# Kernel tuning notes

Hardware: AMD Instinct MI355X
Metric: run time of the kernel (lower is better)

Reference implementation:

```python
import jax, jax.numpy as jnp
import numpy as np

N = 1_000_000
FEAT_DIM = 256
N_CLASS = 345
N_DOMAIN = 6
BETA = 0.5
EPS = 1e-5


def setup_inputs() -> dict:
    key = jax.random.key(0)
    k1, k2, k3, k4 = jax.random.split(key, 4)
    feats = jax.random.normal(k1, (N, FEAT_DIM), dtype=jnp.float32)
    mean = jax.random.normal(k2, (N_DOMAIN, N_CLASS, FEAT_DIM), dtype=jnp.float32)
    amount = jnp.zeros((N_DOMAIN, N_CLASS), dtype=jnp.float32)
    labels = jax.random.randint(k3, (N,), 0, N_CLASS, dtype=jnp.int64 if jax.config.jax_enable_x64 else jnp.int32)
    domains = jax.random.randint(k4, (N,), 0, N_DOMAIN, dtype=jnp.int64 if jax.config.jax_enable_x64 else jnp.int32)
    return {"feats": feats, "mean": mean, "amount": amount,
            "labels": labels, "domains": domains}


def reference(feats, mean, amount, labels, domains):
    # Segmented per-(domain, class) mean of feats. Equivalent to the original
    # onehot broadcast-multiply + sum, but without the O(N*C*F) intermediate.
    seg = domains * N_CLASS + labels  # [N]
    sums = jax.ops.segment_sum(feats, seg, num_segments=N_DOMAIN * N_CLASS)
    sums = sums.reshape(N_DOMAIN, N_CLASS, FEAT_DIM)
    counts = jax.ops.segment_sum(jnp.ones((feats.shape[0],), dtype=feats.dtype), seg,
                                 num_segments=N_DOMAIN * N_CLASS)
    counts = counts.reshape(N_DOMAIN, N_CLASS)

    tmp_mean = sums / (counts[..., None] + EPS)  # [D, C, F]
    # Mask of (domain, class) cells actually observed (tmp_mean row nonzero)
    tmp_mask = (jnp.sum(tmp_mean, axis=-1) != 0).astype(feats.dtype)[..., None]  # [D, C, 1]

    new_mean = mean * (1.0 - tmp_mask) + (mean * BETA + tmp_mean * (1.0 - BETA)) * tmp_mask
    new_amount = jnp.where(counts > 0, jnp.ones_like(amount), amount)
    return new_mean, new_amount
```

## Files before the change

### kernel.cpp

```cpp
#include <hip/hip_runtime.h>
#include <stddef.h>

constexpr int FEAT = 256;
constexpr int F4   = FEAT / 4;
constexpr int NCLS = 345;
constexpr int NDOM = 6;
constexpr int NSEG = NCLS * NDOM;
constexpr int SB   = 256;
constexpr int NTAIL = 22;
constexpr int NFULL = NSEG - NTAIL;
constexpr float BETA = 0.5f;
constexpr float EPS  = 1e-5f;

typedef float f32x4 __attribute__((ext_vector_type(4)));

__global__ void __launch_bounds__(256)
k_hist(const int* __restrict__ labels, const int* __restrict__ domains,
       int n, int chunk, int* __restrict__ W) {
    __shared__ int h[NSEG];
    for (int i = threadIdx.x; i < NSEG; i += blockDim.x) h[i] = 0;
    __syncthreads();
    const int b  = blockIdx.x;
    const int lo = b * chunk;
    const int hi = min(n, lo + chunk);
    for (int i = lo + threadIdx.x; i < hi; i += blockDim.x) {
        int s = domains[i] * NCLS + labels[i];
        atomicAdd(&h[s], 1);
    }
    __syncthreads();
    int* Wb = W + (size_t)b * NSEG;
    for (int i = threadIdx.x; i < NSEG; i += blockDim.x) Wb[i] = h[i];
}

__global__ void __launch_bounds__(256)
k_bases_tot(const int* __restrict__ W, int* __restrict__ Bmat,
            int* __restrict__ totals) {
    const int s = blockIdx.x;
    const int t = threadIdx.x;
    __shared__ int sc[SB];
    int w = W[(size_t)t * NSEG + s];
    sc[t] = w;
    __syncthreads();
    for (int off = 1; off < SB; off <<= 1) {
        int v = (t >= off) ? sc[t - off] : 0;
        __syncthreads();
        sc[t] += v;
        __syncthreads();
    }
    Bmat[(size_t)t * NSEG + s] = sc[t] - w;
    if (t == SB - 1) totals[s] = sc[t];
}

__global__ void k_scan(const int* __restrict__ totals, int* __restrict__ offsets) {
    constexpr int T  = 256;
    constexpr int CH = (NSEG + T - 1) / T;
    __shared__ int csum[T];
    int t = threadIdx.x;
    int base = t * CH;
    int sum = 0;
    for (int j = 0; j < CH; ++j) {
        int idx = base + j;
        if (idx < NSEG) sum += totals[idx];
    }
    csum[t] = sum;
    __syncthreads();
    for (int off = 1; off < T; off <<= 1) {
        int v = (t >= off) ? csum[t - off] : 0;
        __syncthreads();
        csum[t] += v;
        __syncthreads();
    }
    int run = csum[t] - sum;
    for (int j = 0; j < CH; ++j) {
        int idx = base + j;
        if (idx < NSEG) {
            offsets[idx] = run;
            run += totals[idx];
        }
    }
}

__global__ void __launch_bounds__(256)
k_scatter(const int* __restrict__ labels, const int* __restrict__ domains,
          int n, int chunk, const int* __restrict__ Bmat,
          const int* __restrict__ offsets, int* __restrict__ sorted) {
    __shared__ int cur[NSEG];
    const int b = blockIdx.x;
    const int* Bb = Bmat + (size_t)b * NSEG;
    for (int i = threadIdx.x; i < NSEG; i += blockDim.x) cur[i] = Bb[i] + offsets[i];
    __syncthreads();
    const int lo = b * chunk;
    const int hi = min(n, lo + chunk);
    for (int i = lo + threadIdx.x; i < hi; i += blockDim.x) {
        int s = domains[i] * NCLS + labels[i];
        int pos = atomicAdd(&cur[s], 1);
        sorted[pos] = i;
    }
}

__global__ void __launch_bounds__(256)
k_reduce_mixed(const float* __restrict__ feats, const float* __restrict__ mean,
               const float* __restrict__ amount, const int* __restrict__ sorted,
               const int* __restrict__ totals, const int* __restrict__ offsets,
               float* __restrict__ partial, float* __restrict__ out) {
    const int b = blockIdx.x;
    int seg, lo, hi, pslot = 0;
    if (b < NFULL) {
        seg = b;
        lo = 0;
        hi = totals[seg];
    } else {
        const int j  = b - NFULL;
        seg = NFULL + (j >> 2);
        const int q  = j & 3;
        const int cnt = totals[seg];
        const int cq  = (cnt + 3) >> 2;
        lo = min(cnt, q * cq);
        hi = min(cnt, lo + cq);
        pslot = j;
    }
    const int qn   = hi - lo;
    const int base = offsets[seg] + lo;
    const int lane = threadIdx.x & 63;
    const int rp   = threadIdx.x >> 6;

    f32x4 acc = (f32x4)0.0f;
    int r = rp;
    for (; r + 28 < qn; r += 32) {
        int i0 = sorted[base + r];
        int i1 = sorted[base + r + 4];
        int i2 = sorted[base + r + 8];
        int i3 = sorted[base + r + 12];
        int i4 = sorted[base + r + 16];
        int i5 = sorted[base + r + 20];
        int i6 = sorted[base + r + 24];
        int i7 = sorted[base + r + 28];
        f32x4 v0 = reinterpret_cast<const f32x4*>(feats + (size_t)i0 * FEAT)[lane];
        f32x4 v1 = reinterpret_cast<const f32x4*>(feats + (size_t)i1 * FEAT)[lane];
        f32x4 v2 = reinterpret_cast<const f32x4*>(feats + (size_t)i2 * FEAT)[lane];
        f32x4 v3 = reinterpret_cast<const f32x4*>(feats + (size_t)i3 * FEAT)[lane];
        f32x4 v4 = reinterpret_cast<const f32x4*>(feats + (size_t)i4 * FEAT)[lane];
        f32x4 v5 = reinterpret_cast<const f32x4*>(feats + (size_t)i5 * FEAT)[lane];
        f32x4 v6 = reinterpret_cast<const f32x4*>(feats + (size_t)i6 * FEAT)[lane];
        f32x4 v7 = reinterpret_cast<const f32x4*>(feats + (size_t)i7 * FEAT)[lane];
        acc += (v0 + v1) + (v2 + v3) + ((v4 + v5) + (v6 + v7));
    }
    for (; r < qn; r += 4) {
        int i0 = sorted[base + r];
        acc += reinterpret_cast<const f32x4*>(feats + (size_t)i0 * FEAT)[lane];
    }

    __shared__ f32x4 sh[4][F4];
    sh[rp][lane] = acc;
    __syncthreads();
    if (rp == 0) {
        f32x4 s = acc + sh[1][lane] + sh[2][lane] + sh[3][lane];
        if (b < NFULL) {
            const int cnt = hi;
            float inv = 1.0f / ((float)cnt + EPS);
            f32x4 tm = s * inv;
            float lsum = tm.x + tm.y + tm.z + tm.w;
            for (int off = 1; off < 64; off <<= 1) lsum += __shfl_xor(lsum, off, 64);
            bool msk = (lsum != 0.0f);
            f32x4 m4 = reinterpret_cast<const f32x4*>(mean)[(size_t)seg * F4 + lane];
            f32x4 o = msk ? (m4 * BETA + tm * (1.0f - BETA)) : m4;
            reinterpret_cast<f32x4*>(out)[(size_t)seg * F4 + lane] = o;
            if (lane == 0) {
                out[(size_t)NSEG * FEAT + seg] = (cnt > 0) ? 1.0f : amount[seg];
            }
        } else {
            reinterpret_cast<f32x4*>(partial)[(size_t)pslot * F4 + lane] = s;
        }
    }
}

__global__ void k_final_tail(const float* __restrict__ partial, const float* __restrict__ mean,
                             const float* __restrict__ amount, const int* __restrict__ totals,
                             float* __restrict__ out) {
    const int ts   = blockIdx.x;
    const int seg  = NFULL + ts;
    const int lane = threadIdx.x;
    const int cnt  = totals[seg];
    const f32x4* P = reinterpret_cast<const f32x4*>(partial);
    f32x4 s = P[(size_t)(4 * ts + 0) * F4 + lane]
            + P[(size_t)(4 * ts + 1) * F4 + lane]
            + P[(size_t)(4 * ts + 2) * F4 + lane]
            + P[(size_t)(4 * ts + 3) * F4 + lane];
    float inv = 1.0f / ((float)cnt + EPS);
    f32x4 tm = s * inv;

    float lsum = tm.x + tm.y + tm.z + tm.w;
    for (int off = 1; off < 64; off <<= 1) lsum += __shfl_xor(lsum, off, 64);
    bool msk = (lsum != 0.0f);

    f32x4 m4 = reinterpret_cast<const f32x4*>(mean)[(size_t)seg * F4 + lane];
    f32x4 o = msk ? (m4 * BETA + tm * (1.0f - BETA)) : m4;
    reinterpret_cast<f32x4*>(out)[(size_t)seg * F4 + lane] = o;
    if (lane == 0) {
        out[(size_t)NSEG * FEAT + seg] = (cnt > 0) ? 1.0f : amount[seg];
    }
}

__global__ void k_fb_zero(float* __restrict__ out, int total) {
    int stride = gridDim.x * blockDim.x;
    for (int i = blockIdx.x * blockDim.x + threadIdx.x; i < total; i += stride) out[i] = 0.f;
}

__global__ void k_fb_acc(const float* __restrict__ feats, const int* __restrict__ labels,
                         const int* __restrict__ domains, int n, float* __restrict__ out) {
    int lane   = threadIdx.x & 63;
    int gwave  = (blockIdx.x * blockDim.x + threadIdx.x) >> 6;
    int nwaves = (gridDim.x * blockDim.x) >> 6;
    for (int i = gwave; i < n; i += nwaves) {
        int seg = domains[i] * NCLS + labels[i];
        const float4 v = reinterpret_cast<const float4*>(feats + (size_t)i * FEAT)[lane];
        float* dst = out + (size_t)seg * FEAT + lane * 4;
        atomicAdd(dst + 0, v.x);
        atomicAdd(dst + 1, v.y);
        atomicAdd(dst + 2, v.z);
        atomicAdd(dst + 3, v.w);
        if (lane == 0) atomicAdd(out + (size_t)NSEG * FEAT + seg, 1.0f);
    }
}

__global__ void k_fb_epi(const float* __restrict__ mean, const float* __restrict__ amount,
                         float* __restrict__ out) {
    int seg  = blockIdx.x;
    int lane = threadIdx.x;
    float cntf = out[(size_t)NSEG * FEAT + seg];
    float4 s = reinterpret_cast<float4*>(out)[(size_t)seg * F4 + lane];
    float inv = 1.0f / (cntf + EPS);
    float4 tm = make_float4(s.x * inv, s.y * inv, s.z * inv, s.w * inv);
    float lsum = tm.x + tm.y + tm.z + tm.w;
    for (int off = 1; off < 64; off <<= 1) lsum += __shfl_xor(lsum, off, 64);
    bool msk = (lsum != 0.0f);
    float4 m4 = reinterpret_cast<const float4*>(mean)[(size_t)seg * F4 + lane];
    float4 o;
    if (msk) {
        o.x = m4.x * BETA + tm.x * (1.f - BETA);
        o.y = m4.y * BETA + tm.y * (1.f - BETA);
        o.z = m4.z * BETA + tm.z * (1.f - BETA);
        o.w = m4.w * BETA + tm.w * (1.f - BETA);
    } else {
        o = m4;
    }
    reinterpret_cast<float4*>(out)[(size_t)seg * F4 + lane] = o;
    if (lane == 0) {
        out[(size_t)NSEG * FEAT + seg] = (cntf > 0.5f) ? 1.0f : amount[seg];
    }
}

extern "C" void kernel_launch(void* const* d_in, const int* in_sizes, int n_in,
                              void* d_out, int out_size, void* d_ws, size_t ws_size,
                              hipStream_t stream) {
    const float* feats   = (const float*)d_in[0];
    const float* mean    = (const float*)d_in[1];
    const float* amount  = (const float*)d_in[2];
    const int*   labels  = (const int*)d_in[3];
    const int*   domains = (const int*)d_in[4];
    float* out = (float*)d_out;
    const int n = in_sizes[3];
    const int chunk = (n + SB - 1) / SB;

    size_t need = ((size_t)n + (size_t)SB * NSEG * 2
                   + (size_t)4 * NTAIL * FEAT + (size_t)NSEG * 2) * sizeof(int);
    if (ws_size >= need) {
        int*   sorted  = (int*)d_ws;
        int*   W       = sorted + n;
        int*   Bmat    = W + (size_t)SB * NSEG;
        float* partial = (float*)(Bmat + (size_t)SB * NSEG);
        int*   totals  = (int*)(partial + (size_t)4 * NTAIL * FEAT);
        int*   offsets = totals + NSEG;

        k_hist<<<SB, 256, 0, stream>>>(labels, domains, n, chunk, W);
        k_bases_tot<<<NSEG, 256, 0, stream>>>(W, Bmat, totals);
        k_scan<<<1, 256, 0, stream>>>(totals, offsets);
        k_scatter<<<SB, 256, 0, stream>>>(labels, domains, n, chunk, Bmat, offsets, sorted);
        k_reduce_mixed<<<NFULL + 4 * NTAIL, 256, 0, stream>>>(
            feats, mean, amount, sorted, totals, offsets, partial, out);
        k_final_tail<<<NTAIL, 64, 0, stream>>>(partial, mean, amount, totals, out);
    } else {
        int total = NSEG * FEAT + NSEG;
        k_fb_zero<<<(total + 255) / 256, 256, 0, stream>>>(out, total);
        k_fb_acc<<<2048, 256, 0, stream>>>(feats, labels, domains, n, out);
        k_fb_epi<<<NSEG, 64, 0, stream>>>(mean, amount, out);
    }
}
```

Baseline: 236.0 us.

## Fuse histogram, scan and scatter kernels into one persistent kernel with grid barriers

Merges the four preprocessing kernels (histogram, per-segment block-base scan, offsets scan, scatter) into a single 256-block kernel that synchronises through atomic-counter grid barriers, reset by a memset. The per-segment scan now uses wave shuffles over 4 values per lane instead of a shared-memory Hillis-Steele scan with many __syncthreads. Each block redoes the small totals scan locally rather than waiting on a separate single-block kernel. The aim is to cut kernel launch gaps and the heavy synchronisation of the 2070-block scan kernel. The cost is reliance on all 256 blocks being co-resident for the spin barriers, plus an extra memset call.

Result: slower. 299.4 us (+26.9%).

```diff
diff --git a/kernel.cpp b/kernel.cpp
--- a/kernel.cpp
+++ b/kernel.cpp
@@ -14,84 +14,102 @@
 
 typedef float f32x4 __attribute__((ext_vector_type(4)));
 
+__device__ __forceinline__ void grid_barrier(int* cnt, int nblk) {
+    __syncthreads();
+    if (threadIdx.x == 0) {
+        __threadfence();
+        atomicAdd(cnt, 1);
+        while (__hip_atomic_load(cnt, __ATOMIC_ACQUIRE, __HIP_MEMORY_SCOPE_AGENT) < nblk) {}
+        __threadfence();
+    }
+    __syncthreads();
+}
+
 __global__ void __launch_bounds__(256)
-k_hist(const int* __restrict__ labels, const int* __restrict__ domains,
-       int n, int chunk, int* __restrict__ W) {
-    __shared__ int h[NSEG];
-    for (int i = threadIdx.x; i < NSEG; i += blockDim.x) h[i] = 0;
-    __syncthreads();
-    const int b  = blockIdx.x;
+k_pre(const int* __restrict__ labels, const int* __restrict__ domains,
+      int n, int chunk, int* __restrict__ W, int* __restrict__ Bmat,
+      int* __restrict__ totals, int* __restrict__ offsets,
+      int* __restrict__ sorted, int* __restrict__ bar) {
+    __shared__ int cur[NSEG];
+    __shared__ int toff[NSEG];
+    __shared__ int wt[4];
+    const int b = blockIdx.x;
+    const int t = threadIdx.x;
+    const int lane = t & 63;
+    const int wid  = t >> 6;
+
+    for (int i = t; i < NSEG; i += 256) cur[i] = 0;
+    __syncthreads();
     const int lo = b * chunk;
     const int hi = min(n, lo + chunk);
-    for (int i = lo + threadIdx.x; i < hi; i += blockDim.x) {
+    for (int i = lo + t; i < hi; i += 256) {
         int s = domains[i] * NCLS + labels[i];
-        atomicAdd(&h[s], 1);
-    }
-    __syncthreads();
-    int* Wb = W + (size_t)b * NSEG;
-    for (int i = threadIdx.x; i < NSEG; i += blockDim.x) Wb[i] = h[i];
-}
-
-__global__ void __launch_bounds__(256)
-k_bases_tot(const int* __restrict__ W, int* __restrict__ Bmat,
-            int* __restrict__ totals) {
-    const int s = blockIdx.x;
-    const int t = threadIdx.x;
-    __shared__ int sc[SB];
-    int w = W[(size_t)t * NSEG + s];
-    sc[t] = w;
-    __syncthreads();
-    for (int off = 1; off < SB; off <<= 1) {
-        int v = (t >= off) ? sc[t - off] : 0;
-        __syncthreads();
-        sc[t] += v;
-        __syncthreads();
-    }
-    Bmat[(size_t)t * NSEG + s] = sc[t] - w;
-    if (t == SB - 1) totals[s] = sc[t];
-}
-
-__global__ void k_scan(const int* __restrict__ totals, int* __restrict__ offsets) {
-    constexpr int T  = 256;
-    constexpr int CH = (NSEG + T - 1) / T;
-    __shared__ int csum[T];
-    int t = threadIdx.x;
-    int base = t * CH;
+        atomicAdd(&cur[s], 1);
+    }
+    __syncthreads();
+    {
+        int* Wb = W + (size_t)b * NSEG;
+        for (int i = t; i < NSEG; i += 256) Wb[i] = cur[i];
+    }
+
+    grid_barrier(bar + 0, SB);
+
+    for (int s = b + 256 * wid; s < NSEG; s += 1024) {
+        int w0 = W[(size_t)(4 * lane + 0) * NSEG + s];
+        int w1 = W[(size_t)(4 * lane + 1) * NSEG + s];
+        int w2 = W[(size_t)(4 * lane + 2) * NSEG + s];
+        int w3 = W[(size_t)(4 * lane + 3) * NSEG + s];
+        int lsum = w0 + w1 + w2 + w3;
+        int incl = lsum;
+        for (int off = 1; off < 64; off <<= 1) {
+            int v = __shfl_up(incl, off, 64);
+            if (lane >= off) incl += v;
+        }
+        int excl = incl - lsum;
+        Bmat[(size_t)(4 * lane + 0) * NSEG + s] = excl;
+        Bmat[(size_t)(4 * lane + 1) * NSEG + s] = excl + w0;
+        Bmat[(size_t)(4 * lane + 2) * NSEG + s] = excl + w0 + w1;
+        Bmat[(size_t)(4 * lane + 3) * NSEG + s] = excl + w0 + w1 + w2;
+        if (lane == 63) totals[s] = incl;
+    }
+
+    grid_barrier(bar + 1, SB);
+
+    for (int i = t; i < NSEG; i += 256) toff[i] = totals[i];
+    __syncthreads();
+    constexpr int CH = (NSEG + 255) / 256;
+    const int cbase = t * CH;
     int sum = 0;
     for (int j = 0; j < CH; ++j) {
-        int idx = base + j;
-        if (idx < NSEG) sum += totals[idx];
-    }
-    csum[t] = sum;
-    __syncthreads();
-    for (int off = 1; off < T; off <<= 1) {
-        int v = (t >= off) ? csum[t - off] : 0;
-        __syncthreads();
-        csum[t] += v;
-        __syncthreads();
-    }
-    int run = csum[t] - sum;
+        int idx = cbase + j;
+        if (idx < NSEG) sum += toff[idx];
+    }
+    int incl = sum;
+    for (int off = 1; off < 64; off <<= 1) {
+        int v = __shfl_up(incl, off, 64);
+        if (lane >= off) incl += v;
+    }
+    if (lane == 63) wt[wid] = incl;
+    __syncthreads();
+    int base = 0;
+    for (int wjd = 0; wjd < 4; ++wjd) base += (wjd < wid) ? wt[wjd] : 0;
+    int run = base + incl - sum;
     for (int j = 0; j < CH; ++j) {
-        int idx = base + j;
-        if (idx < NSEG) {
-            offsets[idx] = run;
-            run += totals[idx];
+        int idx = cbase + j;
+        if (idx < NSEG) { int v = toff[idx]; toff[idx] = run; run += v; }
+    }
+    __syncthreads();
+
+    {
+        const int* Bb = Bmat + (size_t)b * NSEG;
+        for (int i = t; i < NSEG; i += 256) {
+            cur[i] = Bb[i] + toff[i];
+            if (b == 0) offsets[i] = toff[i];
         }
     }
-}
-
-__global__ void __launch_bounds__(256)
-k_scatter(const int* __restrict__ labels, const int* __restrict__ domains,
-          int n, int chunk, const int* __restrict__ Bmat,
-          const int* __restrict__ offsets, int* __restrict__ sorted) {
-    __shared__ int cur[NSEG];
-    const int b = blockIdx.x;
-    const int* Bb = Bmat + (size_t)b * NSEG;
-    for (int i = threadIdx.x; i < NSEG; i += blockDim.x) cur[i] = Bb[i] + offsets[i];
-    __syncthreads();
-    const int lo = b * chunk;
-    const int hi = min(n, lo + chunk);
-    for (int i = lo + threadIdx.x; i < hi; i += blockDim.x) {
+    __syncthreads();
+
+    for (int i = lo + t; i < hi; i += 256) {
         int s = domains[i] * NCLS + labels[i];
         int pos = atomicAdd(&cur[s], 1);
         sorted[pos] = i;
@@ -263,7 +281,7 @@
     const int chunk = (n + SB - 1) / SB;
 
     size_t need = ((size_t)n + (size_t)SB * NSEG * 2
-                   + (size_t)4 * NTAIL * FEAT + (size_t)NSEG * 2) * sizeof(int);
+                   + (size_t)4 * NTAIL * FEAT + (size_t)NSEG * 2 + 2) * sizeof(int);
     if (ws_size >= need) {
         int*   sorted  = (int*)d_ws;
         int*   W       = sorted + n;
@@ -271,11 +289,11 @@
         float* partial = (float*)(Bmat + (size_t)SB * NSEG);
         int*   totals  = (int*)(partial + (size_t)4 * NTAIL * FEAT);
         int*   offsets = totals + NSEG;
-
-        k_hist<<<SB, 256, 0, stream>>>(labels, domains, n, chunk, W);
-        k_bases_tot<<<NSEG, 256, 0, stream>>>(W, Bmat, totals);
-        k_scan<<<1, 256, 0, stream>>>(totals, offsets);
-        k_scatter<<<SB, 256, 0, stream>>>(labels, domains, n, chunk, Bmat, offsets, sorted);
+        int*   bar     = offsets + NSEG;
+
+        hipMemsetAsync((void*)bar, 0, 2 * sizeof(int), stream);
+        k_pre<<<SB, 256, 0, stream>>>(labels, domains, n, chunk, W, Bmat,
+                                      totals, offsets, sorted, bar);
         k_reduce_mixed<<<NFULL + 4 * NTAIL, 256, 0, stream>>>(
             feats, mean, amount, sorted, totals, offsets, partial, out);
         k_final_tail<<<NTAIL, 64, 0, stream>>>(partial, mean, amount, totals, out);
```

## Fold offset scan into scatter and tail finalize into reduce via last-block counter

Applied to the files above, without the earlier changes.

Removes two small kernel launches. Every scatter block now recomputes the exclusive scan of segment totals in shared memory, and block 0 writes the offsets out. The tail-segment finalize runs inside the reduce kernel: a global atomic counter, reset in k_bases_tot, elects the last tail block to combine the partials. This trades launch overhead and serialization for redundant per-block scan work and a threadfence/atomic handoff.

After: 238.0 us. Within noise of the previous version (+0.8%).

```diff
diff --git a/kernel.cpp b/kernel.cpp
--- a/kernel.cpp
+++ b/kernel.cpp
@@ -34,9 +34,10 @@
 
 __global__ void __launch_bounds__(256)
 k_bases_tot(const int* __restrict__ W, int* __restrict__ Bmat,
-            int* __restrict__ totals) {
+            int* __restrict__ totals, int* __restrict__ done) {
     const int s = blockIdx.x;
     const int t = threadIdx.x;
+    if (s == 0 && t == 0) done[0] = 0;
     __shared__ int sc[SB];
     int w = W[(size_t)t * NSEG + s];
     sc[t] = w;
@@ -51,47 +52,51 @@
     if (t == SB - 1) totals[s] = sc[t];
 }
 
-__global__ void k_scan(const int* __restrict__ totals, int* __restrict__ offsets) {
-    constexpr int T  = 256;
-    constexpr int CH = (NSEG + T - 1) / T;
-    __shared__ int csum[T];
-    int t = threadIdx.x;
-    int base = t * CH;
-    int sum = 0;
-    for (int j = 0; j < CH; ++j) {
-        int idx = base + j;
-        if (idx < NSEG) sum += totals[idx];
-    }
-    csum[t] = sum;
-    __syncthreads();
-    for (int off = 1; off < T; off <<= 1) {
-        int v = (t >= off) ? csum[t - off] : 0;
-        __syncthreads();
-        csum[t] += v;
-        __syncthreads();
-    }
-    int run = csum[t] - sum;
-    for (int j = 0; j < CH; ++j) {
-        int idx = base + j;
-        if (idx < NSEG) {
-            offsets[idx] = run;
-            run += totals[idx];
-        }
-    }
-}
-
 __global__ void __launch_bounds__(256)
 k_scatter(const int* __restrict__ labels, const int* __restrict__ domains,
           int n, int chunk, const int* __restrict__ Bmat,
-          const int* __restrict__ offsets, int* __restrict__ sorted) {
+          const int* __restrict__ totals, int* __restrict__ offsets,
+          int* __restrict__ sorted) {
+    constexpr int CH = (NSEG + 255) / 256;
     __shared__ int cur[NSEG];
+    __shared__ int toff[NSEG];
+    __shared__ int csum[256];
     const int b = blockIdx.x;
+    const int t = threadIdx.x;
+
+    for (int i = t; i < NSEG; i += 256) toff[i] = totals[i];
+    __syncthreads();
+    const int cbase = t * CH;
+    int sum = 0;
+    for (int j = 0; j < CH; ++j) {
+        int idx = cbase + j;
+        if (idx < NSEG) sum += toff[idx];
+    }
+    csum[t] = sum;
+    __syncthreads();
+    for (int off = 1; off < 256; off <<= 1) {
+        int v = (t >= off) ? csum[t - off] : 0;
+        __syncthreads();
+        csum[t] += v;
+        __syncthreads();
+    }
+    int run = csum[t] - sum;
+    for (int j = 0; j < CH; ++j) {
+        int idx = cbase + j;
+        if (idx < NSEG) { int v = toff[idx]; toff[idx] = run; run += v; }
+    }
+    __syncthreads();
+
     const int* Bb = Bmat + (size_t)b * NSEG;
-    for (int i = threadIdx.x; i < NSEG; i += blockDim.x) cur[i] = Bb[i] + offsets[i];
-    __syncthreads();
+    for (int i = t; i < NSEG; i += 256) {
+        cur[i] = Bb[i] + toff[i];
+        if (b == 0) offsets[i] = toff[i];
+    }
+    __syncthreads();
+
     const int lo = b * chunk;
     const int hi = min(n, lo + chunk);
-    for (int i = lo + threadIdx.x; i < hi; i += blockDim.x) {
+    for (int i = lo + t; i < hi; i += 256) {
         int s = domains[i] * NCLS + labels[i];
         int pos = atomicAdd(&cur[s], 1);
         sorted[pos] = i;
@@ -102,7 +107,8 @@
 k_reduce_mixed(const float* __restrict__ feats, const float* __restrict__ mean,
                const float* __restrict__ amount, const int* __restrict__ sorted,
                const int* __restrict__ totals, const int* __restrict__ offsets,
-               float* __restrict__ partial, float* __restrict__ out) {
+               float* __restrict__ partial, int* __restrict__ done,
+               float* __restrict__ out) {
     const int b = blockIdx.x;
     int seg, lo, hi, pslot = 0;
     if (b < NFULL) {
@@ -172,32 +178,40 @@
             reinterpret_cast<f32x4*>(partial)[(size_t)pslot * F4 + lane] = s;
         }
     }
-}
-
-__global__ void k_final_tail(const float* __restrict__ partial, const float* __restrict__ mean,
-                             const float* __restrict__ amount, const int* __restrict__ totals,
-                             float* __restrict__ out) {
-    const int ts   = blockIdx.x;
-    const int seg  = NFULL + ts;
-    const int lane = threadIdx.x;
-    const int cnt  = totals[seg];
-    const f32x4* P = reinterpret_cast<const f32x4*>(partial);
-    f32x4 s = P[(size_t)(4 * ts + 0) * F4 + lane]
-            + P[(size_t)(4 * ts + 1) * F4 + lane]
-            + P[(size_t)(4 * ts + 2) * F4 + lane]
-            + P[(size_t)(4 * ts + 3) * F4 + lane];
-    float inv = 1.0f / ((float)cnt + EPS);
-    f32x4 tm = s * inv;
-
-    float lsum = tm.x + tm.y + tm.z + tm.w;
-    for (int off = 1; off < 64; off <<= 1) lsum += __shfl_xor(lsum, off, 64);
-    bool msk = (lsum != 0.0f);
-
-    f32x4 m4 = reinterpret_cast<const f32x4*>(mean)[(size_t)seg * F4 + lane];
-    f32x4 o = msk ? (m4 * BETA + tm * (1.0f - BETA)) : m4;
-    reinterpret_cast<f32x4*>(out)[(size_t)seg * F4 + lane] = o;
-    if (lane == 0) {
-        out[(size_t)NSEG * FEAT + seg] = (cnt > 0) ? 1.0f : amount[seg];
+
+    if (b >= NFULL) {
+        __syncthreads();
+        __shared__ int s_last;
+        if (threadIdx.x == 0) {
+            __threadfence();
+            int old = atomicAdd(done, 1);
+            s_last = (old == 4 * NTAIL - 1) ? 1 : 0;
+        }
+        __syncthreads();
+        if (s_last) {
+            __threadfence();
+            const int wid = threadIdx.x >> 6;
+            const f32x4* P = reinterpret_cast<const f32x4*>(partial);
+            for (int ts = wid; ts < NTAIL; ts += 4) {
+                const int sg  = NFULL + ts;
+                const int cnt = totals[sg];
+                f32x4 s2 = P[(size_t)(4 * ts + 0) * F4 + lane]
+                         + P[(size_t)(4 * ts + 1) * F4 + lane]
+                         + P[(size_t)(4 * ts + 2) * F4 + lane]
+                         + P[(size_t)(4 * ts + 3) * F4 + lane];
+                float inv = 1.0f / ((float)cnt + EPS);
+                f32x4 tm = s2 * inv;
+                float lsum = tm.x + tm.y + tm.z + tm.w;
+                for (int off = 1; off < 64; off <<= 1) lsum += __shfl_xor(lsum, off, 64);
+                bool msk = (lsum != 0.0f);
+                f32x4 m4 = reinterpret_cast<const f32x4*>(mean)[(size_t)sg * F4 + lane];
+                f32x4 o = msk ? (m4 * BETA + tm * (1.0f - BETA)) : m4;
+                reinterpret_cast<f32x4*>(out)[(size_t)sg * F4 + lane] = o;
+                if (lane == 0) {
+                    out[(size_t)NSEG * FEAT + sg] = (cnt > 0) ? 1.0f : amount[sg];
+                }
+            }
+        }
     }
 }
 
@@ -263,7 +277,7 @@
     const int chunk = (n + SB - 1) / SB;
 
     size_t need = ((size_t)n + (size_t)SB * NSEG * 2
-                   + (size_t)4 * NTAIL * FEAT + (size_t)NSEG * 2) * sizeof(int);
+                   + (size_t)4 * NTAIL * FEAT + (size_t)NSEG * 2 + 1) * sizeof(int);
     if (ws_size >= need) {
         int*   sorted  = (int*)d_ws;
         int*   W       = sorted + n;
@@ -271,14 +285,13 @@
         float* partial = (float*)(Bmat + (size_t)SB * NSEG);
         int*   totals  = (int*)(partial + (size_t)4 * NTAIL * FEAT);
         int*   offsets = totals + NSEG;
+        int*   done    = offsets + NSEG;
 
         k_hist<<<SB, 256, 0, stream>>>(labels, domains, n, chunk, W);
-        k_bases_tot<<<NSEG, 256, 0, stream>>>(W, Bmat, totals);
-        k_scan<<<1, 256, 0, stream>>>(totals, offsets);
-        k_scatter<<<SB, 256, 0, stream>>>(labels, domains, n, chunk, Bmat, offsets, sorted);
+        k_bases_tot<<<NSEG, 256, 0, stream>>>(W, Bmat, totals, done);
+        k_scatter<<<SB, 256, 0, stream>>>(labels, domains, n, chunk, Bmat, totals, offsets, sorted);
         k_reduce_mixed<<<NFULL + 4 * NTAIL, 256, 0, stream>>>(
-            feats, mean, amount, sorted, totals, offsets, partial, out);
-        k_final_tail<<<NTAIL, 64, 0, stream>>>(partial, mean, amount, totals, out);
+            feats, mean, amount, sorted, totals, offsets, partial, done, out);
     } else {
         int total = NSEG * FEAT + NSEG;
         k_fb_zero<<<(total + 255) / 256, 256, 0, stream>>>(out, total);
```
